# Kernel optimization log

Measured on AMD Instinct MI355X. Metric: run time of the kernel, lower is better.

The kernel has to match this reference:

```python
import jax, jax.numpy as jnp
import numpy as np

HIDDEN = 4096
HALF = HIDDEN // 2
NUM_EXPERTS = 64
TOP_K = 8
TEMPERATURE = 1.0


def setup_inputs() -> dict:
    key = jax.random.key(0)
    k_x, k_w1, k_w2 = jax.random.split(key, 3)
    B, S = 4, 4096
    x = jax.random.normal(k_x, (B, S, HIDDEN), dtype=jnp.float32)
    attention_mask = jnp.ones((B, S), dtype=jnp.float32)
    # nn.init.normal_(std=0.02), zero bias
    W1 = 0.02 * jax.random.normal(k_w1, (HIDDEN, HALF), dtype=jnp.float32)
    b1 = jnp.zeros((HALF,), dtype=jnp.float32)
    W2 = 0.02 * jax.random.normal(k_w2, (HALF, NUM_EXPERTS), dtype=jnp.float32)
    b2 = jnp.zeros((NUM_EXPERTS,), dtype=jnp.float32)
    return {"x": x, "attention_mask": attention_mask, "W1": W1, "b1": b1, "W2": W2, "b2": b2}


def reference(x, attention_mask, W1, b1, W2, b2):
    B, S, H = x.shape
    x_flat = x.reshape(-1, H)  # [T, H], T = B*S
    # router MLP (eval mode: dropout is identity, no noise)
    h = jax.nn.gelu(x_flat @ W1 + b1, approximate=False)  # [T, H/2]
    logits = h @ W2 + b2  # [T, E]
    T = logits.shape[0]
    # top-k sparse gating: softmax over selected logits, scatter into dense [T, E]
    top_v, top_i = jax.lax.top_k(logits, TOP_K)  # [T, K]
    top_w = jax.nn.softmax(top_v / TEMPERATURE, axis=-1)  # [T, K]
    weights = jnp.zeros_like(logits).at[jnp.arange(T)[:, None], top_i].set(top_w)
    expert_weights = weights.reshape(B, S, NUM_EXPERTS)
    router_logits = logits.reshape(B, S, NUM_EXPERTS)
    mask = attention_mask[:, :, None].astype(expert_weights.dtype)
    expert_weights = expert_weights * mask
    router_logits = router_logits * mask
    return expert_weights, router_logits
```

## Files before the change

### kernel.cpp

```cpp
#include <hip/hip_runtime.h>
#include <hip/hip_bf16.h>
#include <math.h>

#define HIDDEN 4096
#define HALF   2048
#define NE     64
#define TOPK   8

typedef __attribute__((ext_vector_type(8))) short  short8;
typedef __attribute__((ext_vector_type(4))) float  floatx4;

__device__ inline unsigned short bf16_rne(float v) {
    union { float f; unsigned u; } x; x.f = v;
    unsigned r = x.u + 0x7fffu + ((x.u >> 16) & 1u);
    return (unsigned short)(r >> 16);
}
__device__ inline float bf16_to_f(unsigned short b) {
    union { unsigned u; float f; } x; x.u = (unsigned)b << 16;
    return x.f;
}

__device__ inline void hstore(float* p, float v) { *p = v; }
__device__ inline void hstore(__hip_bfloat16* p, float v) { *p = __float2bfloat16(v); }
__device__ inline float hload(const float* p) { return *p; }
__device__ inline float hload(const __hip_bfloat16* p) { return __bfloat162float(*p); }

template <typename HT>
__global__ __launch_bounds__(256, 2) void gemm1_gelu_mfma(const float* __restrict__ x,
                                                          const float* __restrict__ W1,
                                                          const float* __restrict__ bias1,
                                                          HT* __restrict__ h) {
    __shared__ unsigned short Ah[128][40];
    __shared__ unsigned short Al[128][40];
    __shared__ unsigned short Bh[128][40];
    __shared__ unsigned short Bl[128][40];

    const int tid  = threadIdx.x;
    const int m0   = blockIdx.x * 128;
    const int n0   = blockIdx.y * 128;
    const int wave = tid >> 6, lane = tid & 63;
    const int wm   = (wave & 1) * 64;
    const int wn   = (wave >> 1) * 64;
    const int l15  = lane & 15;
    const int q    = lane >> 4;

    const int sm = tid & 127;
    const int kh = (tid >> 7) * 16;

    floatx4 acc[4][4];
#pragma unroll
    for (int i = 0; i < 4; ++i)
#pragma unroll
        for (int j = 0; j < 4; ++j) acc[i][j] = (floatx4)0.f;

    const float* xp = x  + (size_t)(m0 + sm) * HIDDEN + kh;
    const float* wp = W1 + (size_t)kh * HALF + n0 + sm;

    for (int k0 = 0; k0 < HIDDEN; k0 += 32) {
        float4 av[4];
#pragma unroll
        for (int i = 0; i < 4; ++i) av[i] = *(const float4*)(xp + k0 + i * 4);
        float bv[16];
#pragma unroll
        for (int i = 0; i < 16; ++i) bv[i] = wp[(size_t)(k0 + i) * HALF];

        __syncthreads();

        {
            unsigned short hi[16], lo[16];
#pragma unroll
            for (int i = 0; i < 4; ++i) {
                const float vs[4] = {av[i].x, av[i].y, av[i].z, av[i].w};
#pragma unroll
                for (int j = 0; j < 4; ++j) {
                    float v = vs[j];
                    unsigned short hb = bf16_rne(v);
                    hi[i * 4 + j] = hb;
                    lo[i * 4 + j] = bf16_rne(v - bf16_to_f(hb));
                }
            }
            *(short8*)&Ah[sm][kh]     = *(const short8*)&hi[0];
            *(short8*)&Ah[sm][kh + 8] = *(const short8*)&hi[8];
            *(short8*)&Al[sm][kh]     = *(const short8*)&lo[0];
            *(short8*)&Al[sm][kh + 8] = *(const short8*)&lo[8];
        }
        {
            unsigned short hi[16], lo[16];
#pragma unroll
            for (int i = 0; i < 16; ++i) {
                float v = bv[i];
                unsigned short hb = bf16_rne(v);
                hi[i] = hb;
                lo[i] = bf16_rne(v - bf16_to_f(hb));
            }
            *(short8*)&Bh[sm][kh]     = *(const short8*)&hi[0];
            *(short8*)&Bh[sm][kh + 8] = *(const short8*)&hi[8];
            *(short8*)&Bl[sm][kh]     = *(const short8*)&lo[0];
            *(short8*)&Bl[sm][kh + 8] = *(const short8*)&lo[8];
        }
        __syncthreads();

        short8 a_hi[4], a_lo[4], b_hi[4], b_lo[4];
#pragma unroll
        for (int t = 0; t < 4; ++t) {
            a_hi[t] = *(const short8*)&Ah[wm + t * 16 + l15][q * 8];
            a_lo[t] = *(const short8*)&Al[wm + t * 16 + l15][q * 8];
            b_hi[t] = *(const short8*)&Bh[wn + t * 16 + l15][q * 8];
            b_lo[t] = *(const short8*)&Bl[wn + t * 16 + l15][q * 8];
        }
#pragma unroll
        for (int i = 0; i < 4; ++i)
#pragma unroll
            for (int j = 0; j < 4; ++j) {
                acc[i][j] = __builtin_amdgcn_mfma_f32_16x16x32_bf16(a_hi[i], b_hi[j], acc[i][j], 0, 0, 0);
                acc[i][j] = __builtin_amdgcn_mfma_f32_16x16x32_bf16(a_lo[i], b_hi[j], acc[i][j], 0, 0, 0);
                acc[i][j] = __builtin_amdgcn_mfma_f32_16x16x32_bf16(a_hi[i], b_lo[j], acc[i][j], 0, 0, 0);
            }
    }

#pragma unroll
    for (int j = 0; j < 4; ++j) {
        const int n = n0 + wn + j * 16 + l15;
        const float bb = bias1[n];
#pragma unroll
        for (int i = 0; i < 4; ++i) {
            const int mbase = m0 + wm + i * 16 + q * 4;
#pragma unroll
            for (int r = 0; r < 4; ++r) {
                float v = acc[i][j][r] + bb;
                float g = 0.5f * v * (1.0f + erff(v * 0.70710678118654752f));
                hstore(h + (size_t)(mbase + r) * HALF + n, g);
            }
        }
    }
}

template <typename HT>
__global__ __launch_bounds__(256) void gemm2(const HT* __restrict__ h,
                                             const float* __restrict__ W2,
                                             const float* __restrict__ bias2,
                                             float* __restrict__ logits) {
    __shared__ float hs[HALF];
    __shared__ float red[4][NE];
    const int tid = threadIdx.x;
    const size_t r = blockIdx.x;
    const HT* hr = h + r * HALF;
    for (int i = tid; i < HALF; i += 256) hs[i] = hload(hr + i);
    __syncthreads();
    const int e = tid & 63, qq = tid >> 6;
    float s = 0.f;
    const float* w = W2 + e;
#pragma unroll 8
    for (int k = qq * 512; k < qq * 512 + 512; ++k)
        s = fmaf(hs[k], w[(size_t)k * NE], s);
    red[qq][e] = s;
    __syncthreads();
    if (tid < 64)
        logits[r * NE + tid] = ((red[0][tid] + red[1][tid]) + (red[2][tid] + red[3][tid])) + bias2[tid];
}

__global__ __launch_bounds__(256) void topk_softmax(const float* __restrict__ logits,
                                                    const float* __restrict__ amask,
                                                    float* __restrict__ out, int T) {
    const int wave = threadIdx.x >> 6;
    const int lane = threadIdx.x & 63;
    const int r = blockIdx.x * 4 + wave;
    if (r >= T) return;

    const float v  = logits[(size_t)r * NE + lane];
    const float mk = amask[r];

    out[(size_t)T * NE + (size_t)r * NE + lane] = v * mk;

    bool  sel = false;
    float m0 = 0.f, Z = 0.f;
#pragma unroll
    for (int it = 0; it < TOPK; ++it) {
        float cand = sel ? -INFINITY : v;
        int   idx  = lane;
#pragma unroll
        for (int off = 32; off; off >>= 1) {
            float ov = __shfl_xor(cand, off, 64);
            int   oi = __shfl_xor(idx,  off, 64);
            if (ov > cand || (ov == cand && oi < idx)) { cand = ov; idx = oi; }
        }
        if (it == 0) m0 = cand;
        Z += expf(cand - m0);
        if (lane == idx) sel = true;
    }
    const float w = sel ? (expf(v - m0) / Z) : 0.f;
    out[(size_t)r * NE + lane] = w * mk;
}

extern "C" void kernel_launch(void* const* d_in, const int* in_sizes, int n_in,
                              void* d_out, int out_size, void* d_ws, size_t ws_size,
                              hipStream_t stream) {
    const float* x   = (const float*)d_in[0];
    const float* am  = (const float*)d_in[1];
    const float* W1  = (const float*)d_in[2];
    const float* b1  = (const float*)d_in[3];
    const float* W2  = (const float*)d_in[4];
    const float* b2  = (const float*)d_in[5];
    float* out = (float*)d_out;

    const int T = in_sizes[0] / HIDDEN;

    float* logits = (float*)d_ws;
    const size_t logits_bytes = (size_t)T * NE * sizeof(float);
    const size_t h32_bytes    = (size_t)T * HALF * sizeof(float);

    dim3 g1(T / 128, HALF / 128);

    if (ws_size >= logits_bytes + h32_bytes) {
        float* h = (float*)((char*)d_ws + logits_bytes);
        hipLaunchKernelGGL((gemm1_gelu_mfma<float>), g1, dim3(256), 0, stream, x, W1, b1, h);
        hipLaunchKernelGGL((gemm2<float>), dim3(T), dim3(256), 0, stream, h, W2, b2, logits);
    } else {
        __hip_bfloat16* h = (__hip_bfloat16*)((char*)d_ws + logits_bytes);
        hipLaunchKernelGGL((gemm1_gelu_mfma<__hip_bfloat16>), g1, dim3(256), 0, stream, x, W1, b1, h);
        hipLaunchKernelGGL((gemm2<__hip_bfloat16>), dim3(T), dim3(256), 0, stream, h, W2, b2, logits);
    }
    hipLaunchKernelGGL(topk_softmax, dim3(T / 4), dim3(256), 0, stream, logits, am, out, T);
}
```

Measured before the change: 1.630 ms.

## Presplit x and W1 into bf16 hi/lo and stream tiles via global_load_lds

Adds prepass kernels that split x and a transposed W1 into bf16 hi/lo arrays once per call. The GEMM then loads tiles directly into LDS with global_load_lds instead of converting fp32 in registers inside the K loop. This removes the repeated per-tile conversion and the strided fp32 W1 loads, at the cost of extra global traffic and workspace for the split copies. The unpadded LDS rows may cause bank conflicts, and the path only runs when the workspace is large enough.

```diff
diff --git a/kernel.cpp b/kernel.cpp
--- a/kernel.cpp
+++ b/kernel.cpp
@@ -7,8 +7,9 @@
 #define NE     64
 #define TOPK   8
 
-typedef __attribute__((ext_vector_type(8))) short  short8;
-typedef __attribute__((ext_vector_type(4))) float  floatx4;
+typedef __attribute__((ext_vector_type(8))) short          short8;
+typedef __attribute__((ext_vector_type(4))) float          floatx4;
+typedef __attribute__((ext_vector_type(4))) unsigned short ushort4v;
 
 __device__ inline unsigned short bf16_rne(float v) {
     union { float f; unsigned u; } x; x.f = v;
@@ -24,6 +25,136 @@
 __device__ inline void hstore(__hip_bfloat16* p, float v) { *p = __float2bfloat16(v); }
 __device__ inline float hload(const float* p) { return *p; }
 __device__ inline float hload(const __hip_bfloat16* p) { return __bfloat162float(*p); }
+
+__device__ inline void gl2lds16(const void* g, void* l) {
+    __builtin_amdgcn_global_load_lds(
+        (const __attribute__((address_space(1))) void*)g,
+        (__attribute__((address_space(3))) void*)l, 16, 0, 0);
+}
+
+__global__ __launch_bounds__(256) void split_x_k(const float* __restrict__ x,
+                                                 unsigned short* __restrict__ hi,
+                                                 unsigned short* __restrict__ lo) {
+    const size_t i = ((size_t)blockIdx.x * 256 + threadIdx.x) * 4;
+    float4 v = *(const float4*)(x + i);
+    const float vs[4] = {v.x, v.y, v.z, v.w};
+    ushort4v h4, l4;
+#pragma unroll
+    for (int j = 0; j < 4; ++j) {
+        unsigned short hb = bf16_rne(vs[j]);
+        h4[j] = hb;
+        l4[j] = bf16_rne(vs[j] - bf16_to_f(hb));
+    }
+    *(ushort4v*)(hi + i) = h4;
+    *(ushort4v*)(lo + i) = l4;
+}
+
+__global__ __launch_bounds__(256) void split_wt_k(const float* __restrict__ W1,
+                                                  unsigned short* __restrict__ wh,
+                                                  unsigned short* __restrict__ wl) {
+    __shared__ float tile[64][65];
+    const int tid = threadIdx.x;
+    const int bk = blockIdx.x * 64, bn = blockIdx.y * 64;
+    const int c4 = (tid & 15) * 4, r = tid >> 4;
+#pragma unroll
+    for (int rr = 0; rr < 4; ++rr) {
+        const int row = r + rr * 16;
+        *(float4*)&tile[row][c4] = *(const float4*)&W1[(size_t)(bk + row) * HALF + bn + c4];
+    }
+    __syncthreads();
+#pragma unroll
+    for (int rr = 0; rr < 4; ++rr) {
+        const int n = r + rr * 16;
+        ushort4v h4, l4;
+#pragma unroll
+        for (int j = 0; j < 4; ++j) {
+            float v = tile[c4 + j][n];
+            unsigned short hb = bf16_rne(v);
+            h4[j] = hb;
+            l4[j] = bf16_rne(v - bf16_to_f(hb));
+        }
+        *(ushort4v*)&wh[(size_t)(bn + n) * HIDDEN + bk + c4] = h4;
+        *(ushort4v*)&wl[(size_t)(bn + n) * HIDDEN + bk + c4] = l4;
+    }
+}
+
+__global__ __launch_bounds__(256, 2) void gemm1_gelu_pre(const unsigned short* __restrict__ xh,
+                                                         const unsigned short* __restrict__ xl,
+                                                         const unsigned short* __restrict__ wh,
+                                                         const unsigned short* __restrict__ wl,
+                                                         const float* __restrict__ bias1,
+                                                         float* __restrict__ h) {
+    __shared__ unsigned short Ah[128][32];
+    __shared__ unsigned short Al[128][32];
+    __shared__ unsigned short Bh[128][32];
+    __shared__ unsigned short Bl[128][32];
+
+    const int tid  = threadIdx.x;
+    const int m0   = blockIdx.x * 128;
+    const int n0   = blockIdx.y * 128;
+    const int wave = tid >> 6, lane = tid & 63;
+    const int wm   = (wave & 1) * 64;
+    const int wn   = (wave >> 1) * 64;
+    const int l15  = lane & 15;
+    const int q    = lane >> 4;
+
+    const size_t lrow = (size_t)(lane >> 2);
+    const int    lcol = (lane & 3) * 8;
+    const unsigned short* gp;
+    unsigned short* lp;
+    if (wave == 0)      { gp = xh + (m0 + lrow) * HIDDEN + lcol; lp = &Ah[0][0]; }
+    else if (wave == 1) { gp = xl + (m0 + lrow) * HIDDEN + lcol; lp = &Al[0][0]; }
+    else if (wave == 2) { gp = wh + (n0 + lrow) * HIDDEN + lcol; lp = &Bh[0][0]; }
+    else                { gp = wl + (n0 + lrow) * HIDDEN + lcol; lp = &Bl[0][0]; }
+
+    floatx4 acc[4][4];
+#pragma unroll
+    for (int i = 0; i < 4; ++i)
+#pragma unroll
+        for (int j = 0; j < 4; ++j) acc[i][j] = (floatx4)0.f;
+
+    for (int k0 = 0; k0 < HIDDEN; k0 += 32) {
+        __syncthreads();
+#pragma unroll
+        for (int s = 0; s < 8; ++s)
+            gl2lds16(gp + (size_t)s * 16 * HIDDEN, lp + s * 512);
+        gp += 32;
+        __syncthreads();
+
+        short8 a_hi[4], a_lo[4], b_hi[4], b_lo[4];
+#pragma unroll
+        for (int t = 0; t < 4; ++t) {
+            a_hi[t] = *(const short8*)&Ah[wm + t * 16 + l15][q * 8];
+            a_lo[t] = *(const short8*)&Al[wm + t * 16 + l15][q * 8];
+            b_hi[t] = *(const short8*)&Bh[wn + t * 16 + l15][q * 8];
+            b_lo[t] = *(const short8*)&Bl[wn + t * 16 + l15][q * 8];
+        }
+#pragma unroll
+        for (int i = 0; i < 4; ++i)
+#pragma unroll
+            for (int j = 0; j < 4; ++j) {
+                acc[i][j] = __builtin_amdgcn_mfma_f32_16x16x32_bf16(a_hi[i], b_hi[j], acc[i][j], 0, 0, 0);
+                acc[i][j] = __builtin_amdgcn_mfma_f32_16x16x32_bf16(a_lo[i], b_hi[j], acc[i][j], 0, 0, 0);
+                acc[i][j] = __builtin_amdgcn_mfma_f32_16x16x32_bf16(a_hi[i], b_lo[j], acc[i][j], 0, 0, 0);
+            }
+    }
+
+#pragma unroll
+    for (int j = 0; j < 4; ++j) {
+        const int n = n0 + wn + j * 16 + l15;
+        const float bb = bias1[n];
+#pragma unroll
+        for (int i = 0; i < 4; ++i) {
+            const int mbase = m0 + wm + i * 16 + q * 4;
+#pragma unroll
+            for (int r = 0; r < 4; ++r) {
+                float v = acc[i][j][r] + bb;
+                float g = 0.5f * v * (1.0f + erff(v * 0.70710678118654752f));
+                h[(size_t)(mbase + r) * HALF + n] = g;
+            }
+        }
+    }
+}
 
 template <typename HT>
 __global__ __launch_bounds__(256, 2) void gemm1_gelu_mfma(const float* __restrict__ x,
@@ -43,7 +174,6 @@
     const int wn   = (wave >> 1) * 64;
     const int l15  = lane & 15;
     const int q    = lane >> 4;
-
     const int sm = tid & 127;
     const int kh = (tid >> 7) * 16;
 
@@ -65,7 +195,6 @@
         for (int i = 0; i < 16; ++i) bv[i] = wp[(size_t)(k0 + i) * HALF];
 
         __syncthreads();
-
         {
             unsigned short hi[16], lo[16];
 #pragma unroll
@@ -205,13 +334,29 @@
 
     const int T = in_sizes[0] / HIDDEN;
 
-    float* logits = (float*)d_ws;
     const size_t logits_bytes = (size_t)T * NE * sizeof(float);
     const size_t h32_bytes    = (size_t)T * HALF * sizeof(float);
-
+    const size_t xsplit_bytes = (size_t)T * HIDDEN * 2;
+    const size_t wsplit_bytes = (size_t)HIDDEN * HALF * 2;
+    const size_t need_new = logits_bytes + h32_bytes + 2 * xsplit_bytes + 2 * wsplit_bytes;
+
+    float* logits = (float*)d_ws;
     dim3 g1(T / 128, HALF / 128);
 
-    if (ws_size >= logits_bytes + h32_bytes) {
+    if (ws_size >= need_new) {
+        char* p = (char*)d_ws + logits_bytes;
+        float* h = (float*)p;                     p += h32_bytes;
+        unsigned short* xhp = (unsigned short*)p; p += xsplit_bytes;
+        unsigned short* xlp = (unsigned short*)p; p += xsplit_bytes;
+        unsigned short* whp = (unsigned short*)p; p += wsplit_bytes;
+        unsigned short* wlp = (unsigned short*)p;
+
+        const size_t xN = (size_t)T * HIDDEN;
+        hipLaunchKernelGGL(split_x_k, dim3(xN / (4 * 256)), dim3(256), 0, stream, x, xhp, xlp);
+        hipLaunchKernelGGL(split_wt_k, dim3(HIDDEN / 64, HALF / 64), dim3(256), 0, stream, W1, whp, wlp);
+        hipLaunchKernelGGL(gemm1_gelu_pre, g1, dim3(256), 0, stream, xhp, xlp, whp, wlp, b1, h);
+        hipLaunchKernelGGL((gemm2<float>), dim3(T), dim3(256), 0, stream, h, W2, b2, logits);
+    } else if (ws_size >= logits_bytes + h32_bytes) {
         float* h = (float*)((char*)d_ws + logits_bytes);
         hipLaunchKernelGGL((gemm1_gelu_mfma<float>), g1, dim3(256), 0, stream, x, W1, b1, h);
         hipLaunchKernelGGL((gemm2<float>), dim3(T), dim3(256), 0, stream, h, W2, b2, logits);
```

After: 1.721 ms. 5.6% more time.
